# Performance work log

Hardware: AMD Instinct MI355X
Metric: run time of the kernel (lower is better)

## Reference

```python
import jax, jax.numpy as jnp
import numpy as np

H = 128  # GRU units / embedding dim


def gru_dir(x, mask, W, U, b):
    """Keras GRU (reset_after=True), return final state.
    x: [B,T,D] float, mask: [B,T] bool, W: [D,3H], U: [H,3H], b: [2,3H] (input/recurrent bias).
    Gate order in kernels: z, r, h (Keras convention).
    """
    bi, bh = b[0], b[1]
    xproj = jnp.einsum('btd,dk->btk', x, W) + bi          # [B,T,3H] precomputed input projection
    xproj_t = jnp.transpose(xproj, (1, 0, 2))             # [T,B,3H]
    mask_t = jnp.transpose(mask, (1, 0))                  # [T,B]
    h0 = jnp.zeros((x.shape[0], H), dtype=x.dtype)

    def step(h, inp):
        xp, m = inp                                       # [B,3H], [B]
        hU = h @ U + bh                                   # [B,3H]
        z = jax.nn.sigmoid(xp[:, :H] + hU[:, :H])
        r = jax.nn.sigmoid(xp[:, H:2 * H] + hU[:, H:2 * H])
        hh = jnp.tanh(xp[:, 2 * H:] + r * hU[:, 2 * H:])
        h_new = z * h + (1.0 - z) * hh
        h = jnp.where(m[:, None], h_new, h)               # masked steps carry state
        return h, None

    h_final, _ = jax.lax.scan(step, h0, (xproj_t, mask_t))
    return h_final                                        # [B,H]


def setup_inputs() -> dict:
    key = jax.random.key(0)
    ks = jax.random.split(key, 10)
    B, T, V = 512, 512, 50000
    tokens = jax.random.randint(ks[0], (B, T), 0, V, dtype=jnp.int32)
    s = 0.05
    emb = jax.random.normal(ks[1], (V, H), dtype=jnp.float32) * s
    Wf = jax.random.normal(ks[2], (H, 3 * H), dtype=jnp.float32) * s
    Uf = jax.random.normal(ks[3], (H, 3 * H), dtype=jnp.float32) * s
    bf = jnp.zeros((2, 3 * H), dtype=jnp.float32)
    Wb = jax.random.normal(ks[4], (H, 3 * H), dtype=jnp.float32) * s
    Ub = jax.random.normal(ks[5], (H, 3 * H), dtype=jnp.float32) * s
    bb = jnp.zeros((2, 3 * H), dtype=jnp.float32)
    Wd = jax.random.normal(ks[6], (2 * H, 1), dtype=jnp.float32) * s
    bd = jnp.zeros((1,), dtype=jnp.float32)
    return {"tokens": tokens, "emb": emb, "Wf": Wf, "Uf": Uf, "bf": bf,
            "Wb": Wb, "Ub": Ub, "bb": bb, "Wd": Wd, "bd": bd}


def reference(tokens, emb, Wf, Uf, bf, Wb, Ub, bb, Wd, bd):
    x = emb[tokens]                                       # [B,T,H] embedding lookup
    mask = jnp.any(x != 0.0, axis=-1)                     # Masking(mask_value=0)
    x = x * mask[..., None].astype(x.dtype)               # Masking zeroes masked steps
    h_fwd = gru_dir(x, mask, Wf, Uf, bf)                  # forward direction
    h_bwd = gru_dir(x[:, ::-1, :], mask[:, ::-1], Wb, Ub, bb)  # backward direction (reversed time)
    h = jnp.concatenate([h_fwd, h_bwd], axis=-1)          # [B,2H] concat merge
    return jax.nn.sigmoid(h @ Wd + bd)                    # [B,1]
```

## Files before the change

### kernel.cpp

```cpp
#include <hip/hip_runtime.h>

#define TLEN 512
#define HD 128
#define VOC 50000

typedef float fvec4 __attribute__((ext_vector_type(4)));
typedef int   ivec4 __attribute__((ext_vector_type(4)));
typedef int   ivec8 __attribute__((ext_vector_type(8)));

__device__ __forceinline__ float fsig(float a){
  return __builtin_amdgcn_rcpf(1.f + __builtin_amdgcn_exp2f(-1.44269504f * a));
}

__global__ void emb_cvt8(const float* __restrict__ emb, int* __restrict__ out, int n4){
  int i = blockIdx.x * blockDim.x + threadIdx.x;
  if (i < n4){
    float4 v = *(const float4*)(emb + (size_t)i * 4);
    int p = __builtin_amdgcn_cvt_pk_fp8_f32(16.f * v.x, 16.f * v.y, 0, 0);
    p     = __builtin_amdgcn_cvt_pk_fp8_f32(16.f * v.z, 16.f * v.w, p, 1);
    out[i] = p;
  }
}

__global__ __launch_bounds__(256, 1) void gru_scan(
    const int* __restrict__ tokens, const unsigned char* __restrict__ embq,
    const float* __restrict__ Wf, const float* __restrict__ Uf, const float* __restrict__ bfv,
    const float* __restrict__ Wb, const float* __restrict__ Ub, const float* __restrict__ bbv,
    float* __restrict__ hbuf)
{
  const int tid  = threadIdx.x;
  const int wid  = tid >> 6, lane = tid & 63;
  const int l15  = lane & 15, l4 = lane >> 4;
  const int dir  = blockIdx.x >> 7, grp = blockIdx.x & 127;
  const int c0   = wid * 32 + 2 * l15, c1 = c0 + 1;

  const float* __restrict__ W  = dir ? Wb : Wf;
  const float* __restrict__ U  = dir ? Ub : Uf;
  const float* __restrict__ bv = dir ? bbv : bfv;

  __shared__ __attribute__((aligned(16))) unsigned char hl[98304];

  auto pack8 = [&](const float* M, int col)->ivec8{
    ivec8 q;
#pragma unroll
    for (int w = 0; w < 8; ++w){
      const int k0 = l4 * 32 + w * 4;
      int v = __builtin_amdgcn_cvt_pk_fp8_f32(16.f*M[(k0+0)*384 + col], 16.f*M[(k0+1)*384 + col], 0, 0);
      q[w]  = __builtin_amdgcn_cvt_pk_fp8_f32(16.f*M[(k0+2)*384 + col], 16.f*M[(k0+3)*384 + col], v, 1);
    }
    return q;
  };
  const ivec8 Qz0 = pack8(U, c0), Qr0 = pack8(U, 128 + c0), Qh0 = pack8(U, 256 + c0);
  const ivec8 Qz1 = pack8(U, c1), Qr1 = pack8(U, 128 + c1), Qh1 = pack8(U, 256 + c1);
  const ivec8 Pz0 = pack8(W, c0), Pr0 = pack8(W, 128 + c0), Ph0 = pack8(W, 256 + c0);
  const ivec8 Pz1 = pack8(W, c1), Pr1 = pack8(W, 128 + c1), Ph1 = pack8(W, 256 + c1);

  const float bz0 = bv[c0] + bv[384 + c0], br0 = bv[128 + c0] + bv[384 + 128 + c0];
  const float bx0 = bv[256 + c0],          bu0 = bv[384 + 256 + c0];
  const float bz1 = bv[c1] + bv[384 + c1], br1 = bv[128 + c1] + bv[384 + 128 + c1];
  const float bx1 = bv[256 + c1],          bu1 = bv[384 + 256 + c1];
  const fvec4 CZ0 = {bz0,bz0,bz0,bz0}, CR0 = {br0,br0,br0,br0}, CX0 = {bx0,bx0,bx0,bx0};
  const fvec4 CZ1 = {bz1,bz1,bz1,bz1}, CR1 = {br1,br1,br1,br1}, CX1 = {bx1,bx1,bx1,bx1};
  const fvec4 CU0 = {bu0,bu0,bu0,bu0}, CU1 = {bu1,bu1,bu1,bu1};
  const fvec4 ZF  = {0.f,0.f,0.f,0.f};

  for (int i = tid; i < 2048; i += 256) ((int*)hl)[i] = 0;
  float h0a = 0.f, h0b = 0.f;

  const int  brow = l15 >> 2, srow = l15 & 3;
  const long tbx  = (long)(grp * 4 + brow) * TLEN;
  const int  tb0  = dir ? (TLEN - 1) : 0, tsg = dir ? -1 : 1;
  auto tix = [&](int t){ t = (t > TLEN - 1) ? (TLEN - 1) : t; return tb0 + tsg * t; };
#define XLD(tok) (*(const ivec8*)(embq + (size_t)(tok) * HD + l4 * 32))
#define MFS(A, B, C) __builtin_amdgcn_mfma_scale_f32_16x16x128_f8f6f4(A, B, C, 0, 0, 0, 0x7B7B7B7B, 0, 0x7B7B7B7B)

  fvec4 eZ0, eR0, eX0, eZ1, eR1, eX1, oZ0, oR0, oX0, oZ1, oR1, oX1;
  ivec8 xfa, xfb;
  {
    const int t0 = tokens[tbx + tix(srow)];
    ivec8 xf0 = XLD(t0);
    eZ0 = MFS(xf0, Pz0, CZ0); eR0 = MFS(xf0, Pr0, CR0); eX0 = MFS(xf0, Ph0, CX0);
    eZ1 = MFS(xf0, Pz1, CZ1); eR1 = MFS(xf0, Pr1, CR1); eX1 = MFS(xf0, Ph1, CX1);
    const int t1 = tokens[tbx + tix(4 + srow)];
    xfa = XLD(t1);
  }
  int tok2 = tokens[tbx + tix(8 + srow)];

  const int hrd = l15 * 144 + l4 * 32;
  const int wb  = (4 * l4) * 144 + c0;
  __syncthreads();

#define STEP(S, P, XZ0, XR0, XX0, XZ1, XR1, XX1, WV) { \
    ivec4 alo = *(const ivec4*)&hl[(P) + hrd]; \
    ivec4 ahi = *(const ivec4*)&hl[(P) + hrd + 16]; \
    WV \
    ivec8 af = __builtin_shufflevector(alo, ahi, 0,1,2,3,4,5,6,7); \
    fvec4 aZ0 = MFS(af, Qz0, ZF); \
    fvec4 aR0 = MFS(af, Qr0, ZF); \
    fvec4 aU0 = MFS(af, Qh0, CU0); \
    fvec4 aZ1 = MFS(af, Qz1, ZF); \
    fvec4 aR1 = MFS(af, Qr1, ZF); \
    fvec4 aU1 = MFS(af, Qh1, CU1); \
    float z0 = fsig(XZ0[S] + aZ0[0]); \
    float r0 = fsig(XR0[S] + aR0[0]); \
    float a0 = XX0[S] + r0 * aU0[0]; a0 = fmaxf(a0, -30.f); \
    float y0 = __builtin_amdgcn_exp2f(-2.88539008f * a0); \
    float t0 = (1.f - y0) * __builtin_amdgcn_rcpf(1.f + y0); \
    h0a = t0 + z0 * (h0a - t0); \
    float z1 = fsig(XZ1[S] + aZ1[0]); \
    float r1 = fsig(XR1[S] + aR1[0]); \
    float a1 = XX1[S] + r1 * aU1[0]; a1 = fmaxf(a1, -30.f); \
    float y1 = __builtin_amdgcn_exp2f(-2.88539008f * a1); \
    float t1 = (1.f - y1) * __builtin_amdgcn_rcpf(1.f + y1); \
    h0b = t1 + z1 * (h0b - t1); \
    *(unsigned short*)&hl[((P) ^ 4096) + wb] = \
        (unsigned short)(__builtin_amdgcn_cvt_pk_fp8_f32(16.f * h0a, 16.f * h0b, 0, 0) & 0xffff); \
    asm volatile("s_waitcnt lgkmcnt(0)" ::: "memory"); \
    __builtin_amdgcn_s_barrier(); \
}

  for (int g = 0; g < 128; g += 2){
    STEP(0, 0,    eZ0,eR0,eX0,eZ1,eR1,eX1,
         { oZ0 = MFS(xfa, Pz0, CZ0); oR0 = MFS(xfa, Pr0, CR0);
           xfb = XLD(tok2); tok2 = tokens[tbx + tix(4 * (g + 3) + srow)]; })
    STEP(1, 4096, eZ0,eR0,eX0,eZ1,eR1,eX1,
         { oX0 = MFS(xfa, Ph0, CX0); oZ1 = MFS(xfa, Pz1, CZ1); })
    STEP(2, 0,    eZ0,eR0,eX0,eZ1,eR1,eX1,
         { oR1 = MFS(xfa, Pr1, CR1); oX1 = MFS(xfa, Ph1, CX1); })
    STEP(3, 4096, eZ0,eR0,eX0,eZ1,eR1,eX1, { })
    STEP(0, 0,    oZ0,oR0,oX0,oZ1,oR1,oX1,
         { eZ0 = MFS(xfb, Pz0, CZ0); eR0 = MFS(xfb, Pr0, CR0);
           xfa = XLD(tok2); tok2 = tokens[tbx + tix(4 * (g + 4) + srow)]; })
    STEP(1, 4096, oZ0,oR0,oX0,oZ1,oR1,oX1,
         { eX0 = MFS(xfb, Ph0, CX0); eZ1 = MFS(xfb, Pz1, CZ1); })
    STEP(2, 0,    oZ0,oR0,oX0,oZ1,oR1,oX1,
         { eR1 = MFS(xfb, Pr1, CR1); eX1 = MFS(xfb, Ph1, CX1); })
    STEP(3, 4096, oZ0,oR0,oX0,oZ1,oR1,oX1, { })
  }
#undef STEP
#undef MFS
#undef XLD

  hbuf[(size_t)(grp * 4 + l4) * 256 + dir * 128 + c0] = h0a;
  hbuf[(size_t)(grp * 4 + l4) * 256 + dir * 128 + c1] = h0b;
}

__global__ void head_k(const float* __restrict__ hbuf, const float* __restrict__ Wd,
                       const float* __restrict__ bd, float* __restrict__ out){
  const int wid = threadIdx.x >> 6, lane = threadIdx.x & 63;
  const int b = blockIdx.x * 4 + wid;
  const float* hr = hbuf + (size_t)b * 256;
  float s = 0.f;
#pragma unroll
  for (int j = 0; j < 4; ++j){ const int k = j * 64 + lane; s += hr[k] * Wd[k]; }
#pragma unroll
  for (int off = 32; off > 0; off >>= 1) s += __shfl_down(s, off);
  if (lane == 0) out[b] = 1.f / (1.f + __expf(-(s + bd[0])));
}

extern "C" void kernel_launch(void* const* d_in, const int* in_sizes, int n_in,
                              void* d_out, int out_size, void* d_ws, size_t ws_size,
                              hipStream_t stream){
  const int*   tokens = (const int*)  d_in[0];
  const float* emb    = (const float*)d_in[1];
  const float* Wf     = (const float*)d_in[2];
  const float* Uf     = (const float*)d_in[3];
  const float* bf_    = (const float*)d_in[4];
  const float* Wb     = (const float*)d_in[5];
  const float* Ub     = (const float*)d_in[6];
  const float* bb_    = (const float*)d_in[7];
  const float* Wd     = (const float*)d_in[8];
  const float* bd     = (const float*)d_in[9];
  float* out = (float*)d_out;

  unsigned char* embq = (unsigned char*)d_ws;
  float* hbuf = (float*)((char*)d_ws + (size_t)VOC * HD);

  const int n4 = VOC * HD / 4;
  emb_cvt8<<<(n4 + 255) / 256, 256, 0, stream>>>(emb, (int*)embq, n4);
  gru_scan<<<256, 256, 0, stream>>>(tokens, embq, Wf, Uf, bf_, Wb, Ub, bb_, hbuf);
  head_k<<<128, 256, 0, stream>>>(hbuf, Wd, bd, out);
}
```

Before: 190.7 us.

## Halve batch rows per block, launch twice as many blocks, simplify input-projection pipeline

Each block now handles 2 batch rows instead of 4, and the grid doubles to 512 blocks so more CUs run the serial recurrence at once. The MFMA tile keeps 4 row slots, so half of them hold duplicated rows and that compute is wasted. The double-buffered input projection, spread across steps, is replaced by a single batch of six MFMAs at the end of every fourth step. The recurrent bias moves out of the MFMA accumulator and into a scalar add. Shared memory per block drops to 81920 bytes, but launch_bounds(256,1) and that size probably still allow only one block per CU.

```diff
diff --git a/kernel.cpp b/kernel.cpp
--- a/kernel.cpp
+++ b/kernel.cpp
@@ -31,14 +31,14 @@
   const int tid  = threadIdx.x;
   const int wid  = tid >> 6, lane = tid & 63;
   const int l15  = lane & 15, l4 = lane >> 4;
-  const int dir  = blockIdx.x >> 7, grp = blockIdx.x & 127;
+  const int dir  = blockIdx.x >> 8, grp = blockIdx.x & 255;
   const int c0   = wid * 32 + 2 * l15, c1 = c0 + 1;
 
   const float* __restrict__ W  = dir ? Wb : Wf;
   const float* __restrict__ U  = dir ? Ub : Uf;
   const float* __restrict__ bv = dir ? bbv : bfv;
 
-  __shared__ __attribute__((aligned(16))) unsigned char hl[98304];
+  __shared__ __attribute__((aligned(16))) unsigned char hl[81920];
 
   auto pack8 = [&](const float* M, int col)->ivec8{
     ivec8 q;
@@ -59,30 +59,27 @@
   const float bx0 = bv[256 + c0],          bu0 = bv[384 + 256 + c0];
   const float bz1 = bv[c1] + bv[384 + c1], br1 = bv[128 + c1] + bv[384 + 128 + c1];
   const float bx1 = bv[256 + c1],          bu1 = bv[384 + 256 + c1];
-  const fvec4 CZ0 = {bz0,bz0,bz0,bz0}, CR0 = {br0,br0,br0,br0}, CX0 = {bx0,bx0,bx0,bx0};
-  const fvec4 CZ1 = {bz1,bz1,bz1,bz1}, CR1 = {br1,br1,br1,br1}, CX1 = {bx1,bx1,bx1,bx1};
-  const fvec4 CU0 = {bu0,bu0,bu0,bu0}, CU1 = {bu1,bu1,bu1,bu1};
   const fvec4 ZF  = {0.f,0.f,0.f,0.f};
+#define SP4(b) ((fvec4){(b),(b),(b),(b)})
 
   for (int i = tid; i < 2048; i += 256) ((int*)hl)[i] = 0;
   float h0a = 0.f, h0b = 0.f;
 
-  const int  brow = l15 >> 2, srow = l15 & 3;
-  const long tbx  = (long)(grp * 4 + brow) * TLEN;
+  const int  brow = (l15 >> 2) & 1, srow = l15 & 3;
+  const long tbx  = (long)(grp * 2 + brow) * TLEN;
   const int  tb0  = dir ? (TLEN - 1) : 0, tsg = dir ? -1 : 1;
   auto tix = [&](int t){ t = (t > TLEN - 1) ? (TLEN - 1) : t; return tb0 + tsg * t; };
 #define XLD(tok) (*(const ivec8*)(embq + (size_t)(tok) * HD + l4 * 32))
 #define MFS(A, B, C) __builtin_amdgcn_mfma_scale_f32_16x16x128_f8f6f4(A, B, C, 0, 0, 0, 0x7B7B7B7B, 0, 0x7B7B7B7B)
 
-  fvec4 eZ0, eR0, eX0, eZ1, eR1, eX1, oZ0, oR0, oX0, oZ1, oR1, oX1;
-  ivec8 xfa, xfb;
+  fvec4 xZ0, xR0, xX0, xZ1, xR1, xX1;
+  ivec8 xfa;
   {
     const int t0 = tokens[tbx + tix(srow)];
     ivec8 xf0 = XLD(t0);
-    eZ0 = MFS(xf0, Pz0, CZ0); eR0 = MFS(xf0, Pr0, CR0); eX0 = MFS(xf0, Ph0, CX0);
-    eZ1 = MFS(xf0, Pz1, CZ1); eR1 = MFS(xf0, Pr1, CR1); eX1 = MFS(xf0, Ph1, CX1);
-    const int t1 = tokens[tbx + tix(4 + srow)];
-    xfa = XLD(t1);
+    xZ0 = MFS(xf0, Pz0, SP4(bz0)); xR0 = MFS(xf0, Pr0, SP4(br0)); xX0 = MFS(xf0, Ph0, SP4(bx0));
+    xZ1 = MFS(xf0, Pz1, SP4(bz1)); xR1 = MFS(xf0, Pr1, SP4(br1)); xX1 = MFS(xf0, Ph1, SP4(bx1));
+    xfa = XLD(tokens[tbx + tix(4 + srow)]);
   }
   int tok2 = tokens[tbx + tix(8 + srow)];
 
@@ -90,59 +87,55 @@
   const int wb  = (4 * l4) * 144 + c0;
   __syncthreads();
 
-#define STEP(S, P, XZ0, XR0, XX0, XZ1, XR1, XX1, WV) { \
+#define STEP(S, P, XTRA) { \
     ivec4 alo = *(const ivec4*)&hl[(P) + hrd]; \
     ivec4 ahi = *(const ivec4*)&hl[(P) + hrd + 16]; \
-    WV \
     ivec8 af = __builtin_shufflevector(alo, ahi, 0,1,2,3,4,5,6,7); \
     fvec4 aZ0 = MFS(af, Qz0, ZF); \
     fvec4 aR0 = MFS(af, Qr0, ZF); \
-    fvec4 aU0 = MFS(af, Qh0, CU0); \
+    fvec4 aU0 = MFS(af, Qh0, ZF); \
     fvec4 aZ1 = MFS(af, Qz1, ZF); \
     fvec4 aR1 = MFS(af, Qr1, ZF); \
-    fvec4 aU1 = MFS(af, Qh1, CU1); \
-    float z0 = fsig(XZ0[S] + aZ0[0]); \
-    float r0 = fsig(XR0[S] + aR0[0]); \
-    float a0 = XX0[S] + r0 * aU0[0]; a0 = fmaxf(a0, -30.f); \
+    fvec4 aU1 = MFS(af, Qh1, ZF); \
+    float z0 = fsig(xZ0[S] + aZ0[0]); \
+    float r0 = fsig(xR0[S] + aR0[0]); \
+    float a0 = xX0[S] + r0 * (aU0[0] + bu0); a0 = fmaxf(a0, -30.f); \
     float y0 = __builtin_amdgcn_exp2f(-2.88539008f * a0); \
     float t0 = (1.f - y0) * __builtin_amdgcn_rcpf(1.f + y0); \
     h0a = t0 + z0 * (h0a - t0); \
-    float z1 = fsig(XZ1[S] + aZ1[0]); \
-    float r1 = fsig(XR1[S] + aR1[0]); \
-    float a1 = XX1[S] + r1 * aU1[0]; a1 = fmaxf(a1, -30.f); \
+    float z1 = fsig(xZ1[S] + aZ1[0]); \
+    float r1 = fsig(xR1[S] + aR1[0]); \
+    float a1 = xX1[S] + r1 * (aU1[0] + bu1); a1 = fmaxf(a1, -30.f); \
     float y1 = __builtin_amdgcn_exp2f(-2.88539008f * a1); \
     float t1 = (1.f - y1) * __builtin_amdgcn_rcpf(1.f + y1); \
     h0b = t1 + z1 * (h0b - t1); \
     *(unsigned short*)&hl[((P) ^ 4096) + wb] = \
         (unsigned short)(__builtin_amdgcn_cvt_pk_fp8_f32(16.f * h0a, 16.f * h0b, 0, 0) & 0xffff); \
+    XTRA \
     asm volatile("s_waitcnt lgkmcnt(0)" ::: "memory"); \
     __builtin_amdgcn_s_barrier(); \
 }
 
-  for (int g = 0; g < 128; g += 2){
-    STEP(0, 0,    eZ0,eR0,eX0,eZ1,eR1,eX1,
-         { oZ0 = MFS(xfa, Pz0, CZ0); oR0 = MFS(xfa, Pr0, CR0);
-           xfb = XLD(tok2); tok2 = tokens[tbx + tix(4 * (g + 3) + srow)]; })
-    STEP(1, 4096, eZ0,eR0,eX0,eZ1,eR1,eX1,
-         { oX0 = MFS(xfa, Ph0, CX0); oZ1 = MFS(xfa, Pz1, CZ1); })
-    STEP(2, 0,    eZ0,eR0,eX0,eZ1,eR1,eX1,
-         { oR1 = MFS(xfa, Pr1, CR1); oX1 = MFS(xfa, Ph1, CX1); })
-    STEP(3, 4096, eZ0,eR0,eX0,eZ1,eR1,eX1, { })
-    STEP(0, 0,    oZ0,oR0,oX0,oZ1,oR1,oX1,
-         { eZ0 = MFS(xfb, Pz0, CZ0); eR0 = MFS(xfb, Pr0, CR0);
-           xfa = XLD(tok2); tok2 = tokens[tbx + tix(4 * (g + 4) + srow)]; })
-    STEP(1, 4096, oZ0,oR0,oX0,oZ1,oR1,oX1,
-         { eX0 = MFS(xfb, Ph0, CX0); eZ1 = MFS(xfb, Pz1, CZ1); })
-    STEP(2, 0,    oZ0,oR0,oX0,oZ1,oR1,oX1,
-         { eR1 = MFS(xfb, Pr1, CR1); eX1 = MFS(xfb, Ph1, CX1); })
-    STEP(3, 4096, oZ0,oR0,oX0,oZ1,oR1,oX1, { })
+  for (int g = 0; g < 128; ++g){
+    STEP(0, 0,    { })
+    STEP(1, 4096, { })
+    STEP(2, 0,    { })
+    STEP(3, 4096, {
+      xZ0 = MFS(xfa, Pz0, SP4(bz0)); xR0 = MFS(xfa, Pr0, SP4(br0)); xX0 = MFS(xfa, Ph0, SP4(bx0));
+      xZ1 = MFS(xfa, Pz1, SP4(bz1)); xR1 = MFS(xfa, Pr1, SP4(br1)); xX1 = MFS(xfa, Ph1, SP4(bx1));
+      xfa = XLD(tok2);
+      tok2 = tokens[tbx + tix(4 * (g + 3) + srow)];
+    })
   }
 #undef STEP
 #undef MFS
 #undef XLD
+#undef SP4
 
-  hbuf[(size_t)(grp * 4 + l4) * 256 + dir * 128 + c0] = h0a;
-  hbuf[(size_t)(grp * 4 + l4) * 256 + dir * 128 + c1] = h0b;
+  if (l4 < 2){
+    hbuf[(size_t)(grp * 2 + l4) * 256 + dir * 128 + c0] = h0a;
+    hbuf[(size_t)(grp * 2 + l4) * 256 + dir * 128 + c1] = h0b;
+  }
 }
 
 __global__ void head_k(const float* __restrict__ hbuf, const float* __restrict__ Wd,
@@ -178,6 +171,6 @@
 
   const int n4 = VOC * HD / 4;
   emb_cvt8<<<(n4 + 255) / 256, 256, 0, stream>>>(emb, (int*)embq, n4);
-  gru_scan<<<256, 256, 0, stream>>>(tokens, embq, Wf, Uf, bf_, Wb, Ub, bb_, hbuf);
+  gru_scan<<<512, 256, 0, stream>>>(tokens, embq, Wf, Uf, bf_, Wb, Ub, bb_, hbuf);
   head_k<<<128, 256, 0, stream>>>(hbuf, Wd, bd, out);
 }
```

Measured after the change: 376.7 us. 1.98x slower.
